# Optimization experiments

Measured on AMD Instinct MI355X. Metric: run time of the kernel, lower is better.

Reference implementation:

```python
import jax, jax.numpy as jnp
import numpy as np

N_NODES = 50000
N_EDGES = 800000
IN_CH = 128
HID = 64
HEADS = 4
OUT_CH = 10
N_GRAPHS = 512
NEG_SLOPE = 0.2


def setup_inputs() -> dict:
    key = jax.random.key(0)
    ks = jax.random.split(key, 16)
    x = jax.random.normal(ks[0], (N_NODES, IN_CH), dtype=jnp.float32)
    edge_index = jax.random.randint(ks[1], (2, N_EDGES), 0, N_NODES, dtype=jnp.int64)
    batch = jnp.sort(jax.random.randint(ks[2], (N_NODES,), 0, N_GRAPHS, dtype=jnp.int64))
    s = 1.0 / np.sqrt(IN_CH)
    W1 = jax.random.uniform(ks[3], (IN_CH, HEADS * HID), jnp.float32, -s, s)
    att_src1 = jax.random.normal(ks[4], (HEADS, HID), jnp.float32) * 0.1
    att_dst1 = jax.random.normal(ks[5], (HEADS, HID), jnp.float32) * 0.1
    b1 = jnp.zeros((HEADS * HID,), jnp.float32)
    s2 = 1.0 / np.sqrt(HEADS * HID)
    W2 = jax.random.uniform(ks[6], (HEADS * HID, HID), jnp.float32, -s2, s2)
    att_src2 = jax.random.normal(ks[7], (1, HID), jnp.float32) * 0.1
    att_dst2 = jax.random.normal(ks[8], (1, HID), jnp.float32) * 0.1
    b2 = jnp.zeros((HID,), jnp.float32)
    s3 = 1.0 / np.sqrt(HID)
    Wl = jax.random.uniform(ks[9], (HID, OUT_CH), jnp.float32, -s3, s3)
    bl = jnp.zeros((OUT_CH,), jnp.float32)
    return dict(x=x, edge_index=edge_index, batch=batch,
                W1=W1, att_src1=att_src1, att_dst1=att_dst1, b1=b1,
                W2=W2, att_src2=att_src2, att_dst2=att_dst2, b2=b2,
                Wl=Wl, bl=bl)


def gat_conv(x, src, dst, W, att_src, att_dst, bias, heads, out_ch, concat):
    """PyG GATConv: gather -> per-edge attention -> segment softmax over dst -> scatter-add."""
    n = x.shape[0]
    h = (x @ W).reshape(n, heads, out_ch)            # [N,H,C]
    a_s = jnp.sum(h * att_src, axis=-1)              # [N,H]
    a_d = jnp.sum(h * att_dst, axis=-1)              # [N,H]
    e = jax.nn.leaky_relu(a_s[src] + a_d[dst], NEG_SLOPE)  # [E,H]
    m = jax.ops.segment_max(e, dst, num_segments=n)  # stable softmax per dst
    alpha = jnp.exp(e - m[dst])
    denom = jax.ops.segment_sum(alpha, dst, num_segments=n)
    alpha = alpha / denom[dst]
    out = jax.ops.segment_sum(h[src] * alpha[:, :, None], dst, num_segments=n)  # [N,H,C]
    if concat:
        out = out.reshape(n, heads * out_ch)
    else:
        out = out.mean(axis=1)
    return out + bias


def reference(x, edge_index, batch, W1, att_src1, att_dst1, b1,
              W2, att_src2, att_dst2, b2, Wl, bl):
    n = x.shape[0]
    # PyG GATConv default add_self_loops=True
    loops = jnp.arange(n, dtype=edge_index.dtype)
    src = jnp.concatenate([edge_index[0], loops])
    dst = jnp.concatenate([edge_index[1], loops])

    h = jax.nn.elu(gat_conv(x, src, dst, W1, att_src1, att_dst1, b1, HEADS, HID, True))
    h = jax.nn.elu(gat_conv(h, src, dst, W2, att_src2, att_dst2, b2, 1, HID, False))

    # global_mean_pool
    sums = jax.ops.segment_sum(h, batch, num_segments=N_GRAPHS)
    cnts = jax.ops.segment_sum(jnp.ones((n,), h.dtype), batch, num_segments=N_GRAPHS)
    pooled = sums / jnp.maximum(cnts, 1.0)[:, None]

    return pooled @ Wl + bl
```

## Files before the change

kernel.cpp:

```cpp
#include <hip/hip_runtime.h>
#include <hip/hip_bf16.h>
#include <math.h>

#define N_NODES 50000
#define N_EDGES 800000
#define IN_CH 128
#define HID 64
#define HEADS 4
#define OUT_CH 10
#define N_GRAPHS 512
#define NEG_SLOPE 0.2f

#define ETOT_C (N_EDGES + N_NODES)
#define NPB 128
#define NBUK ((N_NODES + NPB - 1) / NPB)
#define EPB 2048
#define GA ((ETOT_C + EPB - 1) / EPB)
#define GB1 ((N_NODES + 63) / 64)
#define GZ 32

using short8_t = __attribute__((ext_vector_type(8))) short;
using f32x4 = __attribute__((ext_vector_type(4))) float;

__device__ __forceinline__ float b2f(unsigned short u) {
    return __uint_as_float(((unsigned)u) << 16);
}
__device__ __forceinline__ unsigned short f2b(float f) {
    __hip_bfloat16 b = __float2bfloat16(f);
    return *(unsigned short*)&b;
}
__device__ __forceinline__ short f2bs(float f) {
    __hip_bfloat16 b = __float2bfloat16(f);
    return *(short*)&b;
}
__device__ __forceinline__ float lrelu(float x) { return x > 0.f ? x : NEG_SLOPE * x; }

__global__ void convw_k(const float* __restrict__ W1, const float* __restrict__ W2,
                        unsigned short* __restrict__ Wt1, unsigned short* __restrict__ Wt2) {
    int idx = blockIdx.x * 256 + threadIdx.x;
    if (idx < 256 * 128) {
        int n = idx / 128, k = idx % 128;
        Wt1[idx] = f2b(W1[(size_t)k * 256 + n]);
    }
    int j = idx - 256 * 128;
    if (j >= 0 && j < 64 * 256) {
        int n = j / 256, k = j % 256;
        Wt2[j] = f2b(W2[(size_t)k * 64 + n]);
    }
}

__global__ __launch_bounds__(256) void mega1_k(
        const float* __restrict__ X, const unsigned short* __restrict__ Wt,
        unsigned short* __restrict__ Yb,
        const float* __restrict__ asrc, const float* __restrict__ adst,
        float* __restrict__ As, float* __restrict__ Ad, int M,
        const int* __restrict__ dst, unsigned* __restrict__ bcnt,
        const int* __restrict__ batch, float* __restrict__ cntf,
        float* __restrict__ pooled) {
    int b = blockIdx.x;
    if (b < GB1) {
        const int lane = threadIdx.x & 63;
        const int w = threadIdx.x >> 6;
        const int r0 = b * 64 + w * 16;
        const int l15 = lane & 15;
        const int rc = min(r0 + l15, M - 1);
        const int kg = (lane >> 4) * 8;

        f32x4 acc[16] = {};
#pragma unroll
        for (int kc = 0; kc < 4; kc++) {
            int k0 = kc * 32 + kg;
            float4 xa = *(const float4*)&X[(size_t)rc * 128 + k0];
            float4 xb = *(const float4*)&X[(size_t)rc * 128 + k0 + 4];
            short8_t af;
            af[0] = f2bs(xa.x); af[1] = f2bs(xa.y); af[2] = f2bs(xa.z); af[3] = f2bs(xa.w);
            af[4] = f2bs(xb.x); af[5] = f2bs(xb.y); af[6] = f2bs(xb.z); af[7] = f2bs(xb.w);
#pragma unroll
            for (int ct = 0; ct < 16; ct++) {
                int col = ct * 16 + l15;
                short8_t bf = *(const short8_t*)&Wt[(size_t)col * 128 + k0];
                acc[ct] = __builtin_amdgcn_mfma_f32_16x16x32_bf16(af, bf, acc[ct], 0, 0, 0);
            }
        }

        const int rbase = r0 + (lane >> 4) * 4;
#pragma unroll
        for (int reg = 0; reg < 4; reg++) {
            int gr = rbase + reg;
            float s0 = 0.f, s1 = 0.f, s2 = 0.f, s3 = 0.f;
            float d0 = 0.f, d1 = 0.f, d2 = 0.f, d3 = 0.f;
#pragma unroll
            for (int cg = 0; cg < 4; cg++) {
                int c = cg * 16 + l15;
                float v0 = acc[0 * 4 + cg][reg], v1 = acc[1 * 4 + cg][reg];
                float v2 = acc[2 * 4 + cg][reg], v3 = acc[3 * 4 + cg][reg];
                s0 += v0 * asrc[0 * 64 + c]; d0 += v0 * adst[0 * 64 + c];
                s1 += v1 * asrc[1 * 64 + c]; d1 += v1 * adst[1 * 64 + c];
                s2 += v2 * asrc[2 * 64 + c]; d2 += v2 * adst[2 * 64 + c];
                s3 += v3 * asrc[3 * 64 + c]; d3 += v3 * adst[3 * 64 + c];
            }
#pragma unroll
            for (int o = 8; o > 0; o >>= 1) {
                s0 += __shfl_xor(s0, o); d0 += __shfl_xor(d0, o);
                s1 += __shfl_xor(s1, o); d1 += __shfl_xor(d1, o);
                s2 += __shfl_xor(s2, o); d2 += __shfl_xor(d2, o);
                s3 += __shfl_xor(s3, o); d3 += __shfl_xor(d3, o);
            }
            if (l15 == 0 && gr < M) {
                *(float4*)&As[gr * 4] = make_float4(s0, s1, s2, s3);
                *(float4*)&Ad[gr * 4] = make_float4(d0, d1, d2, d3);
            }
        }
#pragma unroll
        for (int reg = 0; reg < 4; reg++) {
            int gr = rbase + reg;
            if (gr >= M) continue;
#pragma unroll
            for (int cg = 0; cg < 4; cg++) {
                int c = cg * 16 + l15;
                ushort4 p;
                p.x = f2b(acc[0 * 4 + cg][reg]);
                p.y = f2b(acc[1 * 4 + cg][reg]);
                p.z = f2b(acc[2 * 4 + cg][reg]);
                p.w = f2b(acc[3 * 4 + cg][reg]);
                *(ushort4*)&Yb[(size_t)gr * 256 + c * 4] = p;
            }
        }
        return;
    }
    b -= GB1;
    if (b < GA) {
        __shared__ unsigned bins[NBUK];
        int t = threadIdx.x;
        for (int i = t; i < NBUK; i += 256) bins[i] = 0;
        __syncthreads();
        int e0 = b * EPB;
        int e1 = min(e0 + EPB, ETOT_C);
        for (int i = e0 + t; i < e1; i += 256) {
            int d = (i < N_EDGES) ? dst[i] : i - N_EDGES;
            atomicAdd(&bins[d >> 7], 1u);
        }
        __syncthreads();
        for (int i = t; i < NBUK; i += 256)
            if (bins[i]) atomicAdd(&bcnt[i], bins[i]);
        return;
    }
    b -= GA;
    if (b < 2) {
        int g = b * 256 + threadIdx.x;
        if (g >= N_GRAPHS) return;
        int lo = 0, hi = N_NODES;
        while (lo < hi) { int mid = (lo + hi) >> 1; if (batch[mid] < g) lo = mid + 1; else hi = mid; }
        int lo2 = lo, hi2 = N_NODES;
        while (lo2 < hi2) { int mid = (lo2 + hi2) >> 1; if (batch[mid] < g + 1) lo2 = mid + 1; else hi2 = mid; }
        cntf[g] = (float)(lo2 - lo);
        return;
    }
    b -= 2;
    int idx = b * 256 + threadIdx.x;
    *(float4*)&pooled[(size_t)idx * 4] = make_float4(0.f, 0.f, 0.f, 0.f);
}

__global__ void scanB_k(const unsigned* __restrict__ bcnt, int* __restrict__ bbase,
                        unsigned* __restrict__ bcur) {
    __shared__ int tmp[512];
    int t = threadIdx.x;
    int v = (t < NBUK) ? (int)bcnt[t] : 0;
    tmp[t] = v;
    __syncthreads();
    for (int o = 1; o < 512; o <<= 1) {
        int u = (t >= o) ? tmp[t - o] : 0;
        __syncthreads();
        tmp[t] += u;
        __syncthreads();
    }
    if (t < NBUK) {
        int ex = tmp[t] - v;
        bbase[t] = ex;
        bcur[t] = (unsigned)ex;
    }
    if (t == NBUK - 1) bbase[NBUK] = tmp[t];
}

__global__ __launch_bounds__(256) void passB_k(const int* __restrict__ src,
                                               const int* __restrict__ dst,
                                               unsigned* __restrict__ bcur,
                                               int2* __restrict__ ebuf) {
    __shared__ unsigned bins[NBUK];
    __shared__ unsigned bbl[NBUK];
    __shared__ int dstash[EPB];
    int b = blockIdx.x;
    int t = threadIdx.x;
    for (int i = t; i < NBUK; i += 256) bins[i] = 0;
    __syncthreads();
    int e0 = b * EPB;
    int e1 = min(e0 + EPB, ETOT_C);
    for (int i = e0 + t; i < e1; i += 256) {
        int d = (i < N_EDGES) ? dst[i] : i - N_EDGES;
        dstash[i - e0] = d;
        atomicAdd(&bins[d >> 7], 1u);
    }
    __syncthreads();
    for (int i = t; i < NBUK; i += 256) {
        bbl[i] = bins[i] ? atomicAdd(&bcur[i], bins[i]) : 0u;
    }
    __syncthreads();
    for (int i = t; i < NBUK; i += 256) bins[i] = 0;
    __syncthreads();
    for (int i = e0 + t; i < e1; i += 256) {
        int d = dstash[i - e0];
        int s = (i < N_EDGES) ? src[i] : i - N_EDGES;
        unsigned r = atomicAdd(&bins[d >> 7], 1u);
        ebuf[bbl[d >> 7] + r] = make_int2(s, d);
    }
}

__global__ __launch_bounds__(256) void passC_k(const int* __restrict__ bbase,
                                               const int2* __restrict__ ebuf,
                                               int* __restrict__ rowptr,
                                               int* __restrict__ csrc) {
    __shared__ int cnt[NPB];
    __shared__ int loc[NPB];
    __shared__ int cur[NPB];
    int b = blockIdx.x;
    int t = threadIdx.x;
    int base = bbase[b], end = bbase[b + 1];
    if (t < NPB) cnt[t] = 0;
    __syncthreads();
    for (int j = base + t; j < end; j += 256) {
        int2 e = ebuf[j];
        atomicAdd(&cnt[e.y & (NPB - 1)], 1);
    }
    __syncthreads();
    if (t < NPB) loc[t] = cnt[t];
    __syncthreads();
    for (int o = 1; o < NPB; o <<= 1) {
        int v = (t < NPB && t >= o) ? loc[t - o] : 0;
        __syncthreads();
        if (t < NPB) loc[t] += v;
        __syncthreads();
    }
    if (t < NPB) {
        int node = b * NPB + t;
        if (node < N_NODES) rowptr[node] = base + loc[t] - cnt[t];
        cur[t] = 0;
    }
    if (b == NBUK - 1 && t == 0) rowptr[N_NODES] = end;
    __syncthreads();
    for (int j = base + t; j < end; j += 256) {
        int2 e = ebuf[j];
        int n = e.y & (NPB - 1);
        int r = atomicAdd(&cur[n], 1);
        csrc[base + loc[n] - cnt[n] + r] = e.x;
    }
}

__global__ __launch_bounds__(256) void mfma_gemm2_k(
        const unsigned short* __restrict__ Xb, const unsigned short* __restrict__ Wt,
        unsigned short* __restrict__ Yb,
        const float* __restrict__ asrc, const float* __restrict__ adst,
        float* __restrict__ As, float* __restrict__ Ad, int M) {
    const int lane = threadIdx.x & 63;
    const int w = threadIdx.x >> 6;
    const int r0 = blockIdx.x * 64 + w * 16;
    const int l15 = lane & 15;
    const int rc = min(r0 + l15, M - 1);
    const int kg = (lane >> 4) * 8;

    f32x4 acc[4] = {};
#pragma unroll
    for (int kc = 0; kc < 8; kc++) {
        int k0 = kc * 32 + kg;
        short8_t af = *(const short8_t*)&Xb[(size_t)rc * 256 + k0];
#pragma unroll
        for (int ct = 0; ct < 4; ct++) {
            int col = ct * 16 + l15;
            short8_t bf = *(const short8_t*)&Wt[(size_t)col * 256 + k0];
            acc[ct] = __builtin_amdgcn_mfma_f32_16x16x32_bf16(af, bf, acc[ct], 0, 0, 0);
        }
    }

    const int rbase = r0 + (lane >> 4) * 4;
#pragma unroll
    for (int reg = 0; reg < 4; reg++) {
        int gr = rbase + reg;
        float sv = 0.f, dv = 0.f;
#pragma unroll
        for (int ct = 0; ct < 4; ct++) {
            int c = ct * 16 + l15;
            float v = acc[ct][reg];
            sv += v * asrc[c];
            dv += v * adst[c];
        }
#pragma unroll
        for (int o = 8; o > 0; o >>= 1) { sv += __shfl_xor(sv, o); dv += __shfl_xor(dv, o); }
        if (l15 == 0 && gr < M) { As[gr] = sv; Ad[gr] = dv; }
        if (gr < M) {
#pragma unroll
            for (int ct = 0; ct < 4; ct++)
                Yb[(size_t)gr * 64 + ct * 16 + l15] = f2b(acc[ct][reg]);
        }
    }
}

__global__ void agg1_k(const int* __restrict__ rowptr, const int* __restrict__ csrc,
                       const float* __restrict__ As, const float* __restrict__ Ad,
                       const __hip_bfloat16* __restrict__ Hb,
                       const float* __restrict__ bias,
                       unsigned short* __restrict__ Outb, int nnodes) {
    __shared__ int ssh[4][64];
    __shared__ float4 wsh[4][64];
    int lane = threadIdx.x & 63;
    int w = threadIdx.x >> 6;
    int node = blockIdx.x * 4 + w;
    int beg = rowptr[node], end = rowptr[node + 1];
    int deg = end - beg;
    const unsigned short* hb = (const unsigned short*)Hb;
    float4 bv = *(const float4*)&Ad[node * 4];
    bool fast = (deg <= 64);
    if (fast) {
        bool act = lane < deg;
        int s = act ? csrc[beg + lane] : 0;
        float4 a = *(const float4*)&As[s * 4];
        float e0 = lrelu(a.x + bv.x), e1 = lrelu(a.y + bv.y);
        float e2 = lrelu(a.z + bv.z), e3 = lrelu(a.w + bv.w);
        if (!act) { e0 = e1 = e2 = e3 = -INFINITY; }
        float m0 = e0, m1 = e1, m2 = e2, m3 = e3;
#pragma unroll
        for (int o = 32; o > 0; o >>= 1) {
            m0 = fmaxf(m0, __shfl_xor(m0, o)); m1 = fmaxf(m1, __shfl_xor(m1, o));
            m2 = fmaxf(m2, __shfl_xor(m2, o)); m3 = fmaxf(m3, __shfl_xor(m3, o));
        }
        float x0 = act ? __expf(e0 - m0) : 0.f;
        float x1 = act ? __expf(e1 - m1) : 0.f;
        float x2 = act ? __expf(e2 - m2) : 0.f;
        float x3 = act ? __expf(e3 - m3) : 0.f;
        float d0 = x0, d1 = x1, d2 = x2, d3 = x3;
#pragma unroll
        for (int o = 32; o > 0; o >>= 1) {
            d0 += __shfl_xor(d0, o); d1 += __shfl_xor(d1, o);
            d2 += __shfl_xor(d2, o); d3 += __shfl_xor(d3, o);
        }
        ssh[w][lane] = s;
        wsh[w][lane] = make_float4(x0 / d0, x1 / d1, x2 / d2, x3 / d3);
    }
    __syncthreads();
    float acc0 = 0.f, acc1 = 0.f, acc2 = 0.f, acc3 = 0.f;
    if (fast) {
        float p0 = 0.f, p1 = 0.f, p2 = 0.f, p3 = 0.f;
        int j = 0;
        for (; j + 4 <= deg; j += 4) {
            int sA = ssh[w][j], sB = ssh[w][j + 1], sC = ssh[w][j + 2], sD = ssh[w][j + 3];
            float4 wA = wsh[w][j], wB = wsh[w][j + 1], wC = wsh[w][j + 2], wD = wsh[w][j + 3];
            ushort4 vA = *(const ushort4*)&hb[(size_t)sA * 256 + lane * 4];
            ushort4 vB = *(const ushort4*)&hb[(size_t)sB * 256 + lane * 4];
            ushort4 vC = *(const ushort4*)&hb[(size_t)sC * 256 + lane * 4];
            ushort4 vD = *(const ushort4*)&hb[(size_t)sD * 256 + lane * 4];
            acc0 += wA.x * b2f(vA.x) + wC.x * b2f(vC.x);
            p0   += wB.x * b2f(vB.x) + wD.x * b2f(vD.x);
            acc1 += wA.y * b2f(vA.y) + wC.y * b2f(vC.y);
            p1   += wB.y * b2f(vB.y) + wD.y * b2f(vD.y);
            acc2 += wA.z * b2f(vA.z) + wC.z * b2f(vC.z);
            p2   += wB.z * b2f(vB.z) + wD.z * b2f(vD.z);
            acc3 += wA.w * b2f(vA.w) + wC.w * b2f(vC.w);
            p3   += wB.w * b2f(vB.w) + wD.w * b2f(vD.w);
        }
        for (; j < deg; j++) {
            int s = ssh[w][j];
            float4 wt = wsh[w][j];
            ushort4 v = *(const ushort4*)&hb[(size_t)s * 256 + lane * 4];
            acc0 += wt.x * b2f(v.x); acc1 += wt.y * b2f(v.y);
            acc2 += wt.z * b2f(v.z); acc3 += wt.w * b2f(v.w);
        }
        acc0 += p0; acc1 += p1; acc2 += p2; acc3 += p3;
    } else {
        float m0 = -INFINITY, m1 = -INFINITY, m2 = -INFINITY, m3 = -INFINITY;
        for (int j = beg + lane; j < end; j += 64) {
            float4 a = *(const float4*)&As[csrc[j] * 4];
            m0 = fmaxf(m0, lrelu(a.x + bv.x)); m1 = fmaxf(m1, lrelu(a.y + bv.y));
            m2 = fmaxf(m2, lrelu(a.z + bv.z)); m3 = fmaxf(m3, lrelu(a.w + bv.w));
        }
#pragma unroll
        for (int o = 32; o > 0; o >>= 1) {
            m0 = fmaxf(m0, __shfl_xor(m0, o)); m1 = fmaxf(m1, __shfl_xor(m1, o));
            m2 = fmaxf(m2, __shfl_xor(m2, o)); m3 = fmaxf(m3, __shfl_xor(m3, o));
        }
        float d0 = 0.f, d1 = 0.f, d2 = 0.f, d3 = 0.f;
        for (int j = beg + lane; j < end; j += 64) {
            float4 a = *(const float4*)&As[csrc[j] * 4];
            d0 += __expf(lrelu(a.x + bv.x) - m0); d1 += __expf(lrelu(a.y + bv.y) - m1);
            d2 += __expf(lrelu(a.z + bv.z) - m2); d3 += __expf(lrelu(a.w + bv.w) - m3);
        }
#pragma unroll
        for (int o = 32; o > 0; o >>= 1) {
            d0 += __shfl_xor(d0, o); d1 += __shfl_xor(d1, o);
            d2 += __shfl_xor(d2, o); d3 += __shfl_xor(d3, o);
        }
        for (int j = beg; j < end; j++) {
            int s = csrc[j];
            float4 a = *(const float4*)&As[s * 4];
            float w0 = __expf(lrelu(a.x + bv.x) - m0) / d0;
            float w1 = __expf(lrelu(a.y + bv.y) - m1) / d1;
            float w2 = __expf(lrelu(a.z + bv.z) - m2) / d2;
            float w3 = __expf(lrelu(a.w + bv.w) - m3) / d3;
            ushort4 v = *(const ushort4*)&hb[(size_t)s * 256 + lane * 4];
            acc0 += w0 * b2f(v.x); acc1 += w1 * b2f(v.y);
            acc2 += w2 * b2f(v.z); acc3 += w3 * b2f(v.w);
        }
    }
    float r0 = acc0 + bias[0 * 64 + lane];
    float r1 = acc1 + bias[1 * 64 + lane];
    float r2 = acc2 + bias[2 * 64 + lane];
    float r3 = acc3 + bias[3 * 64 + lane];
    r0 = r0 > 0.f ? r0 : expm1f(r0);
    r1 = r1 > 0.f ? r1 : expm1f(r1);
    r2 = r2 > 0.f ? r2 : expm1f(r2);
    r3 = r3 > 0.f ? r3 : expm1f(r3);
    size_t base = (size_t)node * 256;
    Outb[base + 0 * 64 + lane] = f2b(r0);
    Outb[base + 1 * 64 + lane] = f2b(r1);
    Outb[base + 2 * 64 + lane] = f2b(r2);
    Outb[base + 3 * 64 + lane] = f2b(r3);
}

__global__ void agg2_k(const int* __restrict__ rowptr, const int* __restrict__ csrc,
                       const float* __restrict__ As, const float* __restrict__ Ad,
                       const __hip_bfloat16* __restrict__ Hb,
                       const float* __restrict__ bias, const int* __restrict__ batch,
                       float* __restrict__ pooled, int nnodes) {
    __shared__ int ssh[4][64];
    __shared__ float wsh[4][64];
    int lane = threadIdx.x & 63;
    int w = threadIdx.x >> 6;
    int node = blockIdx.x * 4 + w;
    int beg = rowptr[node], end = rowptr[node + 1];
    int deg = end - beg;
    const unsigned short* hb = (const unsigned short*)Hb;
    float ad = Ad[node];
    bool fast = (deg <= 64);
    if (fast) {
        bool act = lane < deg;
        int s = act ? csrc[beg + lane] : 0;
        float e = lrelu(As[s] + ad);
        if (!act) e = -INFINITY;
        float m = e;
#pragma unroll
        for (int o = 32; o > 0; o >>= 1) m = fmaxf(m, __shfl_xor(m, o));
        float x = act ? __expf(e - m) : 0.f;
        float d = x;
#pragma unroll
        for (int o = 32; o > 0; o >>= 1) d += __shfl_xor(d, o);
        ssh[w][lane] = s;
        wsh[w][lane] = x / d;
    }
    __syncthreads();
    float acc = 0.f;
    if (fast) {
        float p = 0.f;
        int j = 0;
        for (; j + 4 <= deg; j += 4) {
            int sA = ssh[w][j], sB = ssh[w][j + 1], sC = ssh[w][j + 2], sD = ssh[w][j + 3];
            float wA = wsh[w][j], wB = wsh[w][j + 1], wC = wsh[w][j + 2], wD = wsh[w][j + 3];
            acc += wA * b2f(hb[(size_t)sA * 64 + lane]) + wC * b2f(hb[(size_t)sC * 64 + lane]);
            p   += wB * b2f(hb[(size_t)sB * 64 + lane]) + wD * b2f(hb[(size_t)sD * 64 + lane]);
        }
        for (; j < deg; j++) acc += wsh[w][j] * b2f(hb[(size_t)ssh[w][j] * 64 + lane]);
        acc += p;
    } else {
        float m = -INFINITY;
        for (int j = beg + lane; j < end; j += 64) m = fmaxf(m, lrelu(As[csrc[j]] + ad));
#pragma unroll
        for (int o = 32; o > 0; o >>= 1) m = fmaxf(m, __shfl_xor(m, o));
        float d = 0.f;
        for (int j = beg + lane; j < end; j += 64) d += __expf(lrelu(As[csrc[j]] + ad) - m);
#pragma unroll
        for (int o = 32; o > 0; o >>= 1) d += __shfl_xor(d, o);
        for (int j = beg; j < end; j++) {
            int s = csrc[j];
            float wt = __expf(lrelu(As[s] + ad) - m) / d;
            acc += wt * b2f(hb[(size_t)s * 64 + lane]);
        }
    }
    float v = acc + bias[lane];
    v = v > 0.f ? v : expm1f(v);
    atomicAdd(&pooled[batch[node] * 64 + lane], v);
}

__global__ void final_k(const float* __restrict__ pooled, const float* __restrict__ cnt,
                        const float* __restrict__ Wl, const float* __restrict__ bl,
                        float* __restrict__ out) {
    int g = blockIdx.x;
    int t = threadIdx.x;
    __shared__ float s[64];
    float c = cnt[g];
    c = c > 1.f ? c : 1.f;
    s[t] = pooled[g * 64 + t] / c;
    __syncthreads();
    if (t < OUT_CH) {
        float acc = bl[t];
        for (int k = 0; k < 64; k++) acc += s[k] * Wl[k * OUT_CH + t];
        out[g * OUT_CH + t] = acc;
    }
}

extern "C" void kernel_launch(void* const* d_in, const int* in_sizes, int n_in,
                              void* d_out, int out_size, void* d_ws, size_t ws_size,
                              hipStream_t stream) {
    const float* x    = (const float*)d_in[0];
    const int*   ei   = (const int*)d_in[1];
    const int*   batch= (const int*)d_in[2];
    const float* W1   = (const float*)d_in[3];
    const float* as1  = (const float*)d_in[4];
    const float* ad1  = (const float*)d_in[5];
    const float* b1   = (const float*)d_in[6];
    const float* W2   = (const float*)d_in[7];
    const float* as2  = (const float*)d_in[8];
    const float* ad2  = (const float*)d_in[9];
    const float* b2   = (const float*)d_in[10];
    const float* Wl   = (const float*)d_in[11];
    const float* bl   = (const float*)d_in[12];
    float* out = (float*)d_out;

    const int* src = ei;
    const int* dst = ei + N_EDGES;

    char* ws = (char*)d_ws;
    size_t off = 0;
    auto alloc = [&](size_t bytes) {
        void* p = ws + off;
        off = (off + bytes + 255) & ~((size_t)255);
        return p;
    };
    unsigned short* h1b  = (unsigned short*)alloc((size_t)N_NODES * 256 * 2);
    unsigned short* out1b= (unsigned short*)alloc((size_t)N_NODES * 256 * 2);
    float* As1    = (float*)alloc((size_t)N_NODES * 4 * 4);
    float* Ad1    = (float*)alloc((size_t)N_NODES * 4 * 4);
    float* As2    = (float*)alloc((size_t)N_NODES * 4);
    float* Ad2    = (float*)alloc((size_t)N_NODES * 4);
    int*   rowptr = (int*)  alloc((size_t)(N_NODES + 1) * 4);
    int*   csrc   = (int*)  alloc((size_t)ETOT_C * 4);
    int2*  ebuf   = (int2*) alloc((size_t)ETOT_C * 8);
    unsigned* bcnt= (unsigned*)alloc((size_t)NBUK * 4);
    int*   bbase  = (int*)  alloc((size_t)(NBUK + 1) * 4);
    unsigned* bcur= (unsigned*)alloc((size_t)NBUK * 4);
    unsigned short* Wt1 = (unsigned short*)alloc((size_t)256 * 128 * 2);
    unsigned short* Wt2 = (unsigned short*)alloc((size_t)64 * 256 * 2);
    float* pooled = (float*)alloc((size_t)N_GRAPHS * 64 * 4);
    float* cntf   = (float*)alloc((size_t)N_GRAPHS * 4);
    unsigned short* h2b = h1b;

    hipMemsetAsync(bcnt, 0, (size_t)NBUK * 4, stream);

    convw_k<<<192, 256, 0, stream>>>(W1, W2, Wt1, Wt2);
    mega1_k<<<GB1 + GA + 2 + GZ, 256, 0, stream>>>(
        x, Wt1, h1b, as1, ad1, As1, Ad1, N_NODES,
        dst, bcnt, batch, cntf, pooled);

    scanB_k<<<1, 512, 0, stream>>>(bcnt, bbase, bcur);
    passB_k<<<GA, 256, 0, stream>>>(src, dst, bcur, ebuf);
    passC_k<<<NBUK, 256, 0, stream>>>(bbase, ebuf, rowptr, csrc);

    agg1_k<<<N_NODES / 4, 256, 0, stream>>>(rowptr, csrc, As1, Ad1,
                                            (const __hip_bfloat16*)h1b, b1, out1b, N_NODES);

    mfma_gemm2_k<<<(N_NODES + 63) / 64, 256, 0, stream>>>(out1b, Wt2, h2b, as2, ad2,
                                                          As2, Ad2, N_NODES);
    agg2_k<<<N_NODES / 4, 256, 0, stream>>>(rowptr, csrc, As2, Ad2,
                                            (const __hip_bfloat16*)h2b, b2, batch, pooled, N_NODES);

    final_k<<<N_GRAPHS, 64, 0, stream>>>(pooled, cntf, Wl, bl, out);
}
```

Measured before the change: 219.3 us.

## Regroup preprocessing kernels so GEMM1 runs concurrently with edge bucketing pass

Moves the weight conversion into the first multi-role kernel, alongside the bucket counting, graph counts and pool zeroing. The first-layer GEMM then shares a launch with the edge scatter pass that runs after the scan. This cuts one kernel launch and overlaps the GEMM with the bucketing scatter instead of with the counting pass. The cost is larger per-block shared memory in the fused GEMM kernel, since the scatter branch's dstash array is allocated for every block, which may reduce occupancy for the GEMM blocks.

```diff
diff --git a/kernel.cpp b/kernel.cpp
--- a/kernel.cpp
+++ b/kernel.cpp
@@ -18,6 +18,7 @@
 #define GA ((ETOT_C + EPB - 1) / EPB)
 #define GB1 ((N_NODES + 63) / 64)
 #define GZ 32
+#define GW 192
 
 using short8_t = __attribute__((ext_vector_type(8))) short;
 using f32x4 = __attribute__((ext_vector_type(4))) float;
@@ -35,9 +36,48 @@
 }
 __device__ __forceinline__ float lrelu(float x) { return x > 0.f ? x : NEG_SLOPE * x; }
 
-__global__ void convw_k(const float* __restrict__ W1, const float* __restrict__ W2,
-                        unsigned short* __restrict__ Wt1, unsigned short* __restrict__ Wt2) {
-    int idx = blockIdx.x * 256 + threadIdx.x;
+__global__ __launch_bounds__(256) void megaA_k(
+        const int* __restrict__ dst, unsigned* __restrict__ bcnt,
+        const int* __restrict__ batch, float* __restrict__ cntf,
+        float* __restrict__ pooled,
+        const float* __restrict__ W1, const float* __restrict__ W2,
+        unsigned short* __restrict__ Wt1, unsigned short* __restrict__ Wt2) {
+    int b = blockIdx.x;
+    int t = threadIdx.x;
+    if (b < GA) {
+        __shared__ unsigned bins[NBUK];
+        for (int i = t; i < NBUK; i += 256) bins[i] = 0;
+        __syncthreads();
+        int e0 = b * EPB;
+        int e1 = min(e0 + EPB, ETOT_C);
+        for (int i = e0 + t; i < e1; i += 256) {
+            int d = (i < N_EDGES) ? dst[i] : i - N_EDGES;
+            atomicAdd(&bins[d >> 7], 1u);
+        }
+        __syncthreads();
+        for (int i = t; i < NBUK; i += 256)
+            if (bins[i]) atomicAdd(&bcnt[i], bins[i]);
+        return;
+    }
+    b -= GA;
+    if (b < 2) {
+        int g = b * 256 + t;
+        if (g >= N_GRAPHS) return;
+        int lo = 0, hi = N_NODES;
+        while (lo < hi) { int mid = (lo + hi) >> 1; if (batch[mid] < g) lo = mid + 1; else hi = mid; }
+        int lo2 = lo, hi2 = N_NODES;
+        while (lo2 < hi2) { int mid = (lo2 + hi2) >> 1; if (batch[mid] < g + 1) lo2 = mid + 1; else hi2 = mid; }
+        cntf[g] = (float)(lo2 - lo);
+        return;
+    }
+    b -= 2;
+    if (b < GZ) {
+        int idx = b * 256 + t;
+        *(float4*)&pooled[(size_t)idx * 4] = make_float4(0.f, 0.f, 0.f, 0.f);
+        return;
+    }
+    b -= GZ;
+    int idx = b * 256 + t;
     if (idx < 256 * 128) {
         int n = idx / 128, k = idx % 128;
         Wt1[idx] = f2b(W1[(size_t)k * 256 + n]);
@@ -49,14 +89,34 @@
     }
 }
 
-__global__ __launch_bounds__(256) void mega1_k(
+__global__ void scanB_k(const unsigned* __restrict__ bcnt, int* __restrict__ bbase,
+                        unsigned* __restrict__ bcur) {
+    __shared__ int tmp[512];
+    int t = threadIdx.x;
+    int v = (t < NBUK) ? (int)bcnt[t] : 0;
+    tmp[t] = v;
+    __syncthreads();
+    for (int o = 1; o < 512; o <<= 1) {
+        int u = (t >= o) ? tmp[t - o] : 0;
+        __syncthreads();
+        tmp[t] += u;
+        __syncthreads();
+    }
+    if (t < NBUK) {
+        int ex = tmp[t] - v;
+        bbase[t] = ex;
+        bcur[t] = (unsigned)ex;
+    }
+    if (t == NBUK - 1) bbase[NBUK] = tmp[t];
+}
+
+__global__ __launch_bounds__(256) void megaB_k(
         const float* __restrict__ X, const unsigned short* __restrict__ Wt,
         unsigned short* __restrict__ Yb,
         const float* __restrict__ asrc, const float* __restrict__ adst,
         float* __restrict__ As, float* __restrict__ Ad, int M,
-        const int* __restrict__ dst, unsigned* __restrict__ bcnt,
-        const int* __restrict__ batch, float* __restrict__ cntf,
-        float* __restrict__ pooled) {
+        const int* __restrict__ src, const int* __restrict__ dst,
+        unsigned* __restrict__ bcur, int2* __restrict__ ebuf) {
     int b = blockIdx.x;
     if (b < GB1) {
         const int lane = threadIdx.x & 63;
@@ -129,8 +189,10 @@
         return;
     }
     b -= GB1;
-    if (b < GA) {
+    {
         __shared__ unsigned bins[NBUK];
+        __shared__ unsigned bbl[NBUK];
+        __shared__ int dstash[EPB];
         int t = threadIdx.x;
         for (int i = t; i < NBUK; i += 256) bins[i] = 0;
         __syncthreads();
@@ -138,80 +200,22 @@
         int e1 = min(e0 + EPB, ETOT_C);
         for (int i = e0 + t; i < e1; i += 256) {
             int d = (i < N_EDGES) ? dst[i] : i - N_EDGES;
+            dstash[i - e0] = d;
             atomicAdd(&bins[d >> 7], 1u);
         }
         __syncthreads();
-        for (int i = t; i < NBUK; i += 256)
-            if (bins[i]) atomicAdd(&bcnt[i], bins[i]);
-        return;
-    }
-    b -= GA;
-    if (b < 2) {
-        int g = b * 256 + threadIdx.x;
-        if (g >= N_GRAPHS) return;
-        int lo = 0, hi = N_NODES;
-        while (lo < hi) { int mid = (lo + hi) >> 1; if (batch[mid] < g) lo = mid + 1; else hi = mid; }
-        int lo2 = lo, hi2 = N_NODES;
-        while (lo2 < hi2) { int mid = (lo2 + hi2) >> 1; if (batch[mid] < g + 1) lo2 = mid + 1; else hi2 = mid; }
-        cntf[g] = (float)(lo2 - lo);
-        return;
-    }
-    b -= 2;
-    int idx = b * 256 + threadIdx.x;
-    *(float4*)&pooled[(size_t)idx * 4] = make_float4(0.f, 0.f, 0.f, 0.f);
-}
-
-__global__ void scanB_k(const unsigned* __restrict__ bcnt, int* __restrict__ bbase,
-                        unsigned* __restrict__ bcur) {
-    __shared__ int tmp[512];
-    int t = threadIdx.x;
-    int v = (t < NBUK) ? (int)bcnt[t] : 0;
-    tmp[t] = v;
-    __syncthreads();
-    for (int o = 1; o < 512; o <<= 1) {
-        int u = (t >= o) ? tmp[t - o] : 0;
-        __syncthreads();
-        tmp[t] += u;
-        __syncthreads();
-    }
-    if (t < NBUK) {
-        int ex = tmp[t] - v;
-        bbase[t] = ex;
-        bcur[t] = (unsigned)ex;
-    }
-    if (t == NBUK - 1) bbase[NBUK] = tmp[t];
-}
-
-__global__ __launch_bounds__(256) void passB_k(const int* __restrict__ src,
-                                               const int* __restrict__ dst,
-                                               unsigned* __restrict__ bcur,
-                                               int2* __restrict__ ebuf) {
-    __shared__ unsigned bins[NBUK];
-    __shared__ unsigned bbl[NBUK];
-    __shared__ int dstash[EPB];
-    int b = blockIdx.x;
-    int t = threadIdx.x;
-    for (int i = t; i < NBUK; i += 256) bins[i] = 0;
-    __syncthreads();
-    int e0 = b * EPB;
-    int e1 = min(e0 + EPB, ETOT_C);
-    for (int i = e0 + t; i < e1; i += 256) {
-        int d = (i < N_EDGES) ? dst[i] : i - N_EDGES;
-        dstash[i - e0] = d;
-        atomicAdd(&bins[d >> 7], 1u);
-    }
-    __syncthreads();
-    for (int i = t; i < NBUK; i += 256) {
-        bbl[i] = bins[i] ? atomicAdd(&bcur[i], bins[i]) : 0u;
-    }
-    __syncthreads();
-    for (int i = t; i < NBUK; i += 256) bins[i] = 0;
-    __syncthreads();
-    for (int i = e0 + t; i < e1; i += 256) {
-        int d = dstash[i - e0];
-        int s = (i < N_EDGES) ? src[i] : i - N_EDGES;
-        unsigned r = atomicAdd(&bins[d >> 7], 1u);
-        ebuf[bbl[d >> 7] + r] = make_int2(s, d);
+        for (int i = t; i < NBUK; i += 256) {
+            bbl[i] = bins[i] ? atomicAdd(&bcur[i], bins[i]) : 0u;
+        }
+        __syncthreads();
+        for (int i = t; i < NBUK; i += 256) bins[i] = 0;
+        __syncthreads();
+        for (int i = e0 + t; i < e1; i += 256) {
+            int d = dstash[i - e0];
+            int s = (i < N_EDGES) ? src[i] : i - N_EDGES;
+            unsigned r = atomicAdd(&bins[d >> 7], 1u);
+            ebuf[bbl[d >> 7] + r] = make_int2(s, d);
+        }
     }
 }
 
@@ -551,13 +555,12 @@
 
     hipMemsetAsync(bcnt, 0, (size_t)NBUK * 4, stream);
 
-    convw_k<<<192, 256, 0, stream>>>(W1, W2, Wt1, Wt2);
-    mega1_k<<<GB1 + GA + 2 + GZ, 256, 0, stream>>>(
-        x, Wt1, h1b, as1, ad1, As1, Ad1, N_NODES,
-        dst, bcnt, batch, cntf, pooled);
-
+    megaA_k<<<GA + 2 + GZ + GW, 256, 0, stream>>>(dst, bcnt, batch, cntf, pooled,
+                                                  W1, W2, Wt1, Wt2);
     scanB_k<<<1, 512, 0, stream>>>(bcnt, bbase, bcur);
-    passB_k<<<GA, 256, 0, stream>>>(src, dst, bcur, ebuf);
+
+    megaB_k<<<GB1 + GA, 256, 0, stream>>>(x, Wt1, h1b, as1, ad1, As1, Ad1, N_NODES,
+                                          src, dst, bcur, ebuf);
     passC_k<<<NBUK, 256, 0, stream>>>(bbase, ebuf, rowptr, csrc);
 
     agg1_k<<<N_NODES / 4, 256, 0, stream>>>(rowptr, csrc, As1, Ad1,
```

New measurement: 214.2 us (median of 2 runs). 2.3% less time.
